# Optimization experiments

Measured on AMD Instinct MI355X. Metric: run time of the kernel, lower is better.

Reference implementation:

```python
import jax, jax.numpy as jnp
import numpy as np

NUM_USERS = 100000
NUM_ITEMS = 50000
DIM = 64
LAYERS = 3
K = 1
N_NEGS = 16
NNZ = 2000000
BATCH = 2048
N_TOTAL = NUM_USERS + NUM_ITEMS


def setup_inputs() -> dict:
    key = jax.random.key(0)
    ks = jax.random.split(key, 8)
    return {
        "user_embed": 0.1 * jax.random.normal(ks[0], (NUM_USERS, DIM), dtype=jnp.float32),
        "item_embed": 0.1 * jax.random.normal(ks[1], (NUM_ITEMS, DIM), dtype=jnp.float32),
        "graph_vals": jax.random.uniform(ks[2], (NNZ,), dtype=jnp.float32),
        "graph_rows": jax.random.randint(ks[3], (NNZ,), 0, N_TOTAL, dtype=jnp.int32),
        "graph_cols": jax.random.randint(ks[4], (NNZ,), 0, N_TOTAL, dtype=jnp.int32),
        "user_index": jax.random.randint(ks[5], (BATCH,), 0, NUM_USERS, dtype=jnp.int32),
        "pos_index": jax.random.randint(ks[6], (BATCH,), 0, NUM_ITEMS, dtype=jnp.int32),
        "neg_index": jax.random.randint(ks[7], (BATCH, K * N_NEGS), 0, NUM_ITEMS, dtype=jnp.int32),
    }


def _spmm(vals, rows, cols, x):
    # sparse [N,N] @ dense [N,D] via gather + segment_sum
    return jax.ops.segment_sum(vals[:, None] * x[cols], rows, num_segments=N_TOTAL)


def _aggregate(user_embed, item_embed, graph_vals, graph_rows, graph_cols):
    lambdas = [(l + 1) / (LAYERS + 1) for l in range(LAYERS + 1)]
    e = jnp.concatenate([user_embed, item_embed], axis=0)  # [N, D]
    embeds = [e * lambdas[0]]
    for layer in range(LAYERS):
        e = _spmm(graph_vals, graph_rows, graph_cols, e)
        embeds.append(e * lambdas[layer + 1])
    emb = jnp.stack(embeds, axis=1)  # [N, L+1, D]
    return emb[:NUM_USERS], emb[NUM_USERS:]


def _neg_synth(user_emb, item_emb, user_index, neg_cands, pos_item, key):
    u_e = user_emb[user_index]          # [B, L+1, D]
    p_e = item_emb[pos_item]            # [B, L+1, D]
    n_e = item_emb[neg_cands]           # [B, n_negs, L+1, D]
    seed = jax.random.uniform(key, n_e.shape, dtype=n_e.dtype)
    n_e_ = seed * p_e[:, None] + (1.0 - seed) * n_e            # positive mixing
    scores = jnp.sum(u_e[:, None] * n_e_, axis=-1)             # [B, n_negs, L+1]
    idx = jnp.argmax(scores, axis=1)                            # [B, L+1]
    # select per (batch, layer) the best candidate (hop mixing)
    sel = jnp.take_along_axis(
        jnp.transpose(n_e_, (0, 2, 1, 3)),                      # [B, L+1, n_negs, D]
        idx[:, :, None, None], axis=2).squeeze(2)               # [B, L+1, D]
    return sel


def _pool(e):
    return e.reshape(e.shape[:-2] + (-1,))


def reference(user_embed, item_embed, graph_vals, graph_rows, graph_cols,
              user_index, pos_index, neg_index):
    user_emb, item_emb = _aggregate(user_embed, item_embed,
                                    graph_vals, graph_rows, graph_cols)
    nocon_u_e = user_emb[user_index]    # [B, L+1, D]
    nocon_pos_e = item_emb[pos_index]   # [B, L+1, D]
    key = jax.random.key(42)
    nocon_neg = []
    for k in range(K):
        cands = neg_index[:, k * N_NEGS:(k + 1) * N_NEGS]
        nocon_neg.append(_neg_synth(user_emb, item_emb, user_index, cands,
                                    pos_index, jax.random.fold_in(key, k)))
    nocon_neg_e = jnp.stack(nocon_neg, axis=1)  # [B, K, L+1, D]

    u_e = _pool(nocon_u_e)       # [B, (L+1)*D]
    pos_e = _pool(nocon_pos_e)
    neg_e = _pool(nocon_neg_e)   # [B, K, (L+1)*D]

    B = user_index.shape[0]
    reg_loss = 0.5 * (jnp.sum(nocon_u_e[:, 0, :] ** 2)
                      + jnp.sum(nocon_pos_e[:, 0, :] ** 2)
                      + jnp.sum(nocon_neg_e[:, :, 0, :] ** 2)) / float(B)

    pos_scores = jnp.sum(u_e * pos_e, axis=1)                 # [B]
    neg_scores = jnp.sum(u_e[:, None] * neg_e, axis=-1)       # [B, K]
    loss1 = jnp.mean(jnp.log(1.0 + jnp.sum(
        jnp.exp(neg_scores - pos_scores[:, None]), axis=1)))
    return (loss1, reg_loss)
```

## Files before the change

### kernel.cpp

```cpp
#include <hip/hip_runtime.h>

static constexpr int kNumUsers  = 100000;
static constexpr int kNumItems  = 50000;
static constexpr int kNTotal    = 150000;
static constexpr int kDim       = 64;
static constexpr int kNnz       = 2000000;
static constexpr int kBatch     = 2048;
static constexpr int kNeg       = 16;
static constexpr int kRowsPerBucket = 256;
static constexpr int kNumBuckets  = (kNTotal + kRowsPerBucket - 1) / kRowsPerBucket;
static constexpr int kBucketCap   = 4096;
static constexpr int kChunk       = 4096;
static constexpr int kEdgesPerThread = kChunk / 512;
static constexpr int kCurStride   = 16;
static constexpr int kMaxList     = 2048 + 2048 + kBatch * kNeg;
static constexpr unsigned kSeedHalf = 4194304u;

typedef float f32x2 __attribute__((ext_vector_type(2)));


__device__ __forceinline__ unsigned short f2bf(float f) {
  unsigned u = __float_as_uint(f);
  unsigned r = (u + 0x7FFFu + ((u >> 16) & 1u)) >> 16;
  return (unsigned short)r;
}
__device__ __forceinline__ float bf2f(unsigned short h) {
  return __uint_as_float((unsigned)h << 16);
}


struct KeyPair { unsigned a, b; };

constexpr KeyPair tf2x32_const(unsigned k0, unsigned k1, unsigned x0, unsigned x1) {
  unsigned ks[3] = {k0, k1, k0 ^ k1 ^ 0x1BD11BDAu};
  const unsigned rots[2][4] = {{13u,15u,26u,6u},{17u,29u,16u,24u}};
  x0 += ks[0]; x1 += ks[1];
  for (int g = 0; g < 5; ++g) {
    for (int i = 0; i < 4; ++i) {
      unsigned r = rots[g & 1][i];
      x0 += x1;
      x1 = (x1 << r) | (x1 >> (32u - r));
      x1 ^= x0;
    }
    x0 += ks[(g + 1) % 3];
    x1 += ks[(g + 2) % 3] + (unsigned)(g + 1);
  }
  return {x0, x1};
}

static constexpr KeyPair kFoldedKey = tf2x32_const(0u, 42u, 0u, 0u);

__device__ __forceinline__ unsigned rotl32(unsigned x, unsigned r) {
  return (x << r) | (x >> (32u - r));
}

__device__ __forceinline__ void tf2x32(unsigned k0, unsigned k1,
                                       unsigned x0, unsigned x1,
                                       unsigned& y0, unsigned& y1) {
  const unsigned ks2 = k0 ^ k1 ^ 0x1BD11BDAu;
  x0 += k0; x1 += k1;
#define TF_ROUND(r) { x0 += x1; x1 = rotl32(x1, (r)); x1 ^= x0; }
  TF_ROUND(13u) TF_ROUND(15u) TF_ROUND(26u) TF_ROUND(6u)
  x0 += k1;  x1 += ks2 + 1u;
  TF_ROUND(17u) TF_ROUND(29u) TF_ROUND(16u) TF_ROUND(24u)
  x0 += ks2; x1 += k0 + 2u;
  TF_ROUND(13u) TF_ROUND(15u) TF_ROUND(26u) TF_ROUND(6u)
  x0 += k0;  x1 += k1 + 3u;
  TF_ROUND(17u) TF_ROUND(29u) TF_ROUND(16u) TF_ROUND(24u)
  x0 += k1;  x1 += ks2 + 4u;
  TF_ROUND(13u) TF_ROUND(15u) TF_ROUND(26u) TF_ROUND(6u)
  x0 += ks2; x1 += k0 + 5u;
#undef TF_ROUND
  y0 = x0; y1 = x1;
}

__device__ __forceinline__ float bits2f(unsigned bits) {
  return __uint_as_float((bits >> 9) | 0x3F800000u) - 1.0f;
}

__device__ __forceinline__ float wred(float v) {
  for (int o = 32; o; o >>= 1) v += __shfl_xor(v, o, 64);
  return v;
}


__global__ void k_zeroinit(const float* __restrict__ ue, const float* __restrict__ ie,
                           unsigned* __restrict__ e0f8, int* __restrict__ cursor,
                           int* __restrict__ nrows, int* __restrict__ flags) {
  int i = blockIdx.x * blockDim.x + threadIdx.x;
  if (i < kNTotal * 16) {
    const float4* __restrict__ s4 = (i < kNumUsers * 16)
      ? ((const float4*)ue + i)
      : ((const float4*)ie + (i - kNumUsers * 16));
    float4 v = *s4;
    unsigned w = 0;
    w = __builtin_amdgcn_cvt_pk_fp8_f32(v.x, v.y, w, false);
    w = __builtin_amdgcn_cvt_pk_fp8_f32(v.z, v.w, w, true);
    e0f8[i] = w;
  }
  if (i < kNTotal) flags[i] = 0;
  if (i < kNumBuckets) cursor[i * kCurStride] = i * kBucketCap;
  if (i == 0) *nrows = 0;
}

__global__ void __launch_bounds__(512)
k_bscatter(const int* __restrict__ rows, const int* __restrict__ cols,
           const float* __restrict__ vals, int* __restrict__ cursor,
           int2* __restrict__ edges) {
  __shared__ int hist[kNumBuckets];
  __shared__ int base[kNumBuckets];
  int c0 = blockIdx.x * kChunk;

  int   er[kEdgesPerThread];
  int   ec[kEdgesPerThread];
  float ev[kEdgesPerThread];
  int n = 0;
#pragma unroll
  for (int i = 0; i < kEdgesPerThread; ++i) {
    int e = c0 + i * 512 + threadIdx.x;
    if (e < kNnz) {
      er[n] = rows[e];
      ec[n] = cols[e];
      ev[n] = vals[e];
      ++n;
    }
  }

  for (int i = threadIdx.x; i < kNumBuckets; i += 512) hist[i] = 0;
  __syncthreads();
  for (int i = 0; i < n; ++i) atomicAdd(&hist[er[i] >> 8], 1);
  __syncthreads();
  for (int i = threadIdx.x; i < kNumBuckets; i += 512) {
    int c = hist[i];
    base[i] = c ? atomicAdd(&cursor[i * kCurStride], c) : 0;
    hist[i] = 0;
  }
  __syncthreads();
  for (int i = 0; i < n; ++i) {
    int r = er[i];
    int b = r >> 8;
    int p = base[b] + atomicAdd(&hist[b], 1);
    if (p < (b + 1) * kBucketCap) {
      int2 pk;
      pk.x = ec[i] | ((r & 255) << 18);
      pk.y = __float_as_int(ev[i]);
      edges[p] = pk;
    }
  }
}

__global__ void __launch_bounds__(256)
k_bucket_csr(const int2* __restrict__ edges, const int* __restrict__ cursor,
             int2* __restrict__ edges2, int* __restrict__ rbeg, int* __restrict__ rend) {
  __shared__ int cnts[kRowsPerBucket];
  __shared__ int offs[kRowsPerBucket];
  __shared__ int wsum[4];
  int b = blockIdx.x;
  int lo = b * kBucketCap;
  int cnt = cursor[b * kCurStride] - lo; if (cnt > kBucketCap) cnt = kBucketCap;

  cnts[threadIdx.x] = 0;
  __syncthreads();
  for (int e = threadIdx.x; e < cnt; e += 256)
    atomicAdd(&cnts[(edges[lo + e].x >> 18) & 255], 1);
  __syncthreads();

  {
    int tid = threadIdx.x;
    int v = cnts[tid];
    int s = v;
    for (int o = 1; o < 64; o <<= 1) {
      int t = __shfl_up(s, o, 64);
      if ((tid & 63) >= o) s += t;
    }
    if ((tid & 63) == 63) wsum[tid >> 6] = s;
    __syncthreads();
    int woff = 0;
    for (int ww = 0; ww < (tid >> 6); ++ww) woff += wsum[ww];
    int excl = woff + s - v;
    offs[tid] = excl;
    int row = (b << 8) + tid;
    if (row < kNTotal) {
      rbeg[row] = lo + excl;
      rend[row] = lo + excl + v;
    }
  }
  __syncthreads();

  for (int e = threadIdx.x; e < cnt; e += 256) {
    int2 pk = edges[lo + e];
    int rl = (pk.x >> 18) & 255;
    int p = atomicAdd(&offs[rl], 1);
    edges2[lo + p] = make_int2(pk.x & 0x3FFFF, pk.y);
  }
}

__global__ void k_flaglist(const int* __restrict__ uidx, const int* __restrict__ pidx,
                           const int* __restrict__ nidx, int* __restrict__ flags,
                           int* __restrict__ rowlist, int* __restrict__ nrows) {
  int i = blockIdx.x * blockDim.x + threadIdx.x;
  int node = -1;
  if (i < kBatch) node = uidx[i];
  else if (i < 2 * kBatch) node = kNumUsers + pidx[i - kBatch];
  else if (i < 2 * kBatch + kBatch * kNeg) node = kNumUsers + nidx[i - 2 * kBatch];
  if (node >= 0 && atomicExch(&flags[node], 1) == 0) {
    int p = atomicAdd(nrows, 1);
    rowlist[p] = node;
  }
}

#define FMA8(d, v) {                                                      \
    f32x2 q0 = __builtin_amdgcn_cvt_pk_f32_fp8((d).x, false);             \
    f32x2 q1 = __builtin_amdgcn_cvt_pk_f32_fp8((d).x, true);              \
    f32x2 q2 = __builtin_amdgcn_cvt_pk_f32_fp8((d).y, false);             \
    f32x2 q3 = __builtin_amdgcn_cvt_pk_f32_fp8((d).y, true);              \
    a[0] += (v) * q0.x; a[1] += (v) * q0.y; a[2] += (v) * q1.x;           \
    a[3] += (v) * q1.y; a[4] += (v) * q2.x; a[5] += (v) * q2.y;           \
    a[6] += (v) * q3.x; a[7] += (v) * q3.y; }

__device__ __forceinline__ void spmm_row8(int row, int ln,
                                          const int* __restrict__ rbeg,
                                          const int* __restrict__ rend,
                                          const int2* __restrict__ edges2,
                                          const uint2* __restrict__ src8,
                                          unsigned short* __restrict__ dstbf,
                                          uint2* __restrict__ dstf8, int wb) {
  int s = rbeg[row], t = rend[row];
  float a[8];
#pragma unroll
  for (int i = 0; i < 8; ++i) a[i] = 0.0f;
  int e = s;
  for (; e + 3 < t; e += 4) {
    int2 p0 = edges2[e],     p1 = edges2[e + 1];
    int2 p2 = edges2[e + 2], p3 = edges2[e + 3];
    uint2 d0 = src8[(size_t)p0.x * 8 + ln];
    uint2 d1 = src8[(size_t)p1.x * 8 + ln];
    uint2 d2 = src8[(size_t)p2.x * 8 + ln];
    uint2 d3 = src8[(size_t)p3.x * 8 + ln];
    FMA8(d0, __int_as_float(p0.y))
    FMA8(d1, __int_as_float(p1.y))
    FMA8(d2, __int_as_float(p2.y))
    FMA8(d3, __int_as_float(p3.y))
  }
  if (e + 1 < t) {
    int2 p0 = edges2[e], p1 = edges2[e + 1];
    uint2 d0 = src8[(size_t)p0.x * 8 + ln];
    uint2 d1 = src8[(size_t)p1.x * 8 + ln];
    FMA8(d0, __int_as_float(p0.y))
    FMA8(d1, __int_as_float(p1.y))
    e += 2;
  }
  if (e < t) {
    int2 p0 = edges2[e];
    uint2 d0 = src8[(size_t)p0.x * 8 + ln];
    FMA8(d0, __int_as_float(p0.y))
  }
  if (wb) {
    uint4 ob;
    ob.x = (unsigned)f2bf(a[0]) | ((unsigned)f2bf(a[1]) << 16);
    ob.y = (unsigned)f2bf(a[2]) | ((unsigned)f2bf(a[3]) << 16);
    ob.z = (unsigned)f2bf(a[4]) | ((unsigned)f2bf(a[5]) << 16);
    ob.w = (unsigned)f2bf(a[6]) | ((unsigned)f2bf(a[7]) << 16);
    *(uint4*)(dstbf + ((size_t)row << 6) + (ln << 3)) = ob;
  }
  if (dstf8) {
    uint2 o8;
    o8.x = 0; o8.y = 0;
    o8.x = __builtin_amdgcn_cvt_pk_fp8_f32(a[0], a[1], o8.x, false);
    o8.x = __builtin_amdgcn_cvt_pk_fp8_f32(a[2], a[3], o8.x, true);
    o8.y = __builtin_amdgcn_cvt_pk_fp8_f32(a[4], a[5], o8.y, false);
    o8.y = __builtin_amdgcn_cvt_pk_fp8_f32(a[6], a[7], o8.y, true);
    dstf8[(size_t)row * 8 + ln] = o8;
  }
}

__global__ void __launch_bounds__(256)
k_spmm_all(const int* __restrict__ rbeg, const int* __restrict__ rend,
           const int2* __restrict__ edges2, const uint2* __restrict__ src8,
           unsigned short* __restrict__ dstbf, uint2* __restrict__ dstf8,
           const int* __restrict__ flags) {
  int row = blockIdx.x * 32 + (threadIdx.x >> 3);
  if (row >= kNTotal) return;
  spmm_row8(row, threadIdx.x & 7, rbeg, rend, edges2, src8, dstbf, dstf8,
            flags[row]);
}

__global__ void __launch_bounds__(256)
k_spmm_list(const int* __restrict__ rbeg, const int* __restrict__ rend,
            const int2* __restrict__ edges2, const uint2* __restrict__ src8,
            unsigned short* __restrict__ dstbf, const int* __restrict__ rowlist,
            const int* __restrict__ nrows) {
  int gid = blockIdx.x * 32 + (threadIdx.x >> 3);
  if (gid >= *nrows) return;
  spmm_row8(rowlist[gid], threadIdx.x & 7, rbeg, rend, edges2, src8, dstbf,
            nullptr, 1);
}

__global__ void __launch_bounds__(256)
k_batch(const float* __restrict__ ue, const float* __restrict__ ie,
        const unsigned short* __restrict__ e1, const unsigned short* __restrict__ e2,
        const unsigned short* __restrict__ e3, const int* __restrict__ uidx,
        const int* __restrict__ pidx, const int* __restrict__ nidx,
        float2* __restrict__ bout) {
  const float LAM[4] = {0.25f, 0.5f, 0.75f, 1.0f};
  int b0 = blockIdx.x;
  int b1 = b0 + kBatch / 2;
  int lane = threadIdx.x & 63;
  int w = threadIdx.x >> 6;

  __shared__ float s_score[2][kNeg][4];
  __shared__ float s_sq0[2][kNeg];
  __shared__ float s_pos[2], s_usq[2], s_psq[2];

  int un0 = uidx[b0], pi0 = pidx[b0];
  int un1 = uidx[b1], pi1 = pidx[b1];
  size_t uo0 = ((size_t)un0 << 6) + lane, po0 = ((size_t)(kNumUsers + pi0) << 6) + lane;
  size_t uo1 = ((size_t)un1 << 6) + lane, po1 = ((size_t)(kNumUsers + pi1) << 6) + lane;
  float u0[4], p0[4], u1[4], p1[4];
  u0[0] = ue[uo0] * LAM[0]; p0[0] = ie[((size_t)pi0 << 6) + lane] * LAM[0];
  u1[0] = ue[uo1] * LAM[0]; p1[0] = ie[((size_t)pi1 << 6) + lane] * LAM[0];
  u0[1] = bf2f(e1[uo0]) * LAM[1]; p0[1] = bf2f(e1[po0]) * LAM[1];
  u1[1] = bf2f(e1[uo1]) * LAM[1]; p1[1] = bf2f(e1[po1]) * LAM[1];
  u0[2] = bf2f(e2[uo0]) * LAM[2]; p0[2] = bf2f(e2[po0]) * LAM[2];
  u1[2] = bf2f(e2[uo1]) * LAM[2]; p1[2] = bf2f(e2[po1]) * LAM[2];
  u0[3] = bf2f(e3[uo0]) * LAM[3]; p0[3] = bf2f(e3[po0]) * LAM[3];
  u1[3] = bf2f(e3[uo1]) * LAM[3]; p1[3] = bf2f(e3[po1]) * LAM[3];

  if (w == 0) {
    float ps = wred(u0[0]*p0[0] + u0[1]*p0[1] + u0[2]*p0[2] + u0[3]*p0[3]);
    float uq = wred(u0[0] * u0[0]);
    float pq = wred(p0[0] * p0[0]);
    if (lane == 0) { s_pos[0] = ps; s_usq[0] = uq; s_psq[0] = pq; }
  } else if (w == 1) {
    float ps = wred(u1[0]*p1[0] + u1[1]*p1[1] + u1[2]*p1[2] + u1[3]*p1[3]);
    float uq = wred(u1[0] * u1[0]);
    float pq = wred(p1[0] * p1[0]);
    if (lane == 0) { s_pos[1] = ps; s_usq[1] = uq; s_psq[1] = pq; }
  }

#pragma unroll
  for (int j = 0; j < 4; ++j) {
    int c = w * 4 + j;
    int ni0 = nidx[b0 * kNeg + c];
    int ni1 = nidx[b1 * kNeg + c];
    size_t no0 = ((size_t)(kNumUsers + ni0) << 6) + lane;
    size_t no1 = ((size_t)(kNumUsers + ni1) << 6) + lane;
#pragma unroll
    for (int l = 0; l < 4; ++l) {
      float nv0, nv1;
      if (l == 0) {
        nv0 = ie[((size_t)ni0 << 6) + lane] * LAM[0];
        nv1 = ie[((size_t)ni1 << 6) + lane] * LAM[0];
      } else if (l == 1) { nv0 = bf2f(e1[no0]) * LAM[1]; nv1 = bf2f(e1[no1]) * LAM[1]; }
      else if (l == 2)   { nv0 = bf2f(e2[no0]) * LAM[2]; nv1 = bf2f(e2[no1]) * LAM[2]; }
      else               { nv0 = bf2f(e3[no0]) * LAM[3]; nv1 = bf2f(e3[no1]) * LAM[3]; }
      unsigned si = ((unsigned)(b0 * kNeg + c) * 4u + (unsigned)l) * 64u + (unsigned)lane;
      unsigned y0, y1;
      tf2x32(kFoldedKey.a, kFoldedKey.b, si, si + kSeedHalf, y0, y1);
      float sd0 = bits2f(y0);
      float sd1 = bits2f(y1);
      float nm0 = sd0 * p0[l] + (1.0f - sd0) * nv0;
      float nm1 = sd1 * p1[l] + (1.0f - sd1) * nv1;
      float sc0 = wred(u0[l] * nm0);
      float sc1 = wred(u1[l] * nm1);
      if (l == 0) {
        float q0 = wred(nm0 * nm0);
        float q1 = wred(nm1 * nm1);
        if (lane == 0) { s_sq0[0][c] = q0; s_sq0[1][c] = q1; }
      }
      if (lane == 0) { s_score[0][c][l] = sc0; s_score[1][c][l] = sc1; }
    }
  }
  __syncthreads();

  if (w < 2) {
    int c = lane & 15, l = lane >> 4;
    float v = s_score[w][c][l];
    int idx = c;
#pragma unroll
    for (int o = 1; o < 16; o <<= 1) {
      float ov = __shfl_xor(v, o, 64);
      int oi = __shfl_xor(idx, o, 64);
      bool take = (ov > v) || (ov == v && oi < idx);
      v = take ? ov : v;
      idx = take ? oi : idx;
    }
    float sum = v;
    sum += __shfl_xor(sum, 16, 64);
    sum += __shfl_xor(sum, 32, 64);
    if (lane == 0) {
      float x = sum - s_pos[w];
      float term = logf(1.0f + expf(x));
      float reg = 0.5f * (s_usq[w] + s_psq[w] + s_sq0[w][idx]);
      bout[w == 0 ? b0 : b1] = make_float2(term, reg);
    }
  }
}

__global__ void __launch_bounds__(256)
k_reduce(const float2* __restrict__ bout, float* __restrict__ out) {
  float t = 0.0f, r = 0.0f;
  for (int i = threadIdx.x; i < kBatch; i += 256) {
    float2 v = bout[i];
    t += v.x; r += v.y;
  }
  t = wred(t); r = wred(r);
  __shared__ float st[4], sr[4];
  int w = threadIdx.x >> 6;
  if ((threadIdx.x & 63) == 0) { st[w] = t; sr[w] = r; }
  __syncthreads();
  if (threadIdx.x == 0) {
    out[0] = (st[0] + st[1] + st[2] + st[3]) / (float)kBatch;
    out[1] = (sr[0] + sr[1] + sr[2] + sr[3]) / (float)kBatch;
  }
}


extern "C" void kernel_launch(void* const* d_in, const int* in_sizes, int n_in,
                              void* d_out, int out_size, void* d_ws, size_t ws_size,
                              hipStream_t stream) {
  const float* ue   = (const float*)d_in[0];
  const float* ie   = (const float*)d_in[1];
  const float* gv   = (const float*)d_in[2];
  const int*   gr   = (const int*)d_in[3];
  const int*   gc   = (const int*)d_in[4];
  const int*   uidx = (const int*)d_in[5];
  const int*   pidx = (const int*)d_in[6];
  const int*   nidx = (const int*)d_in[7];
  float* out = (float*)d_out;

  char* ws = (char*)d_ws;
  size_t off = 0;
  auto alloc = [&](size_t bytes) -> void* {
    off = (off + 255) & ~(size_t)255;
    void* p = ws + off;
    off += bytes;
    return p;
  };
  const size_t tblElems = (size_t)kNTotal * kDim;
  unsigned*       e0f8 = (unsigned*)      alloc(tblElems);
  unsigned short* e1bf = (unsigned short*)alloc(tblElems * 2);
  uint2*          e1f8 = (uint2*)         alloc(tblElems);
  unsigned short* e2bf = (unsigned short*)alloc(tblElems * 2);
  uint2*          e2f8 = (uint2*)         alloc(tblElems);
  unsigned short* e3bf = (unsigned short*)alloc(tblElems * 2);
  int2* edges   = (int2*)alloc((size_t)kNumBuckets * kBucketCap * sizeof(int2));
  int2* edges2  = (int2*)alloc((size_t)kNumBuckets * kBucketCap * sizeof(int2));
  int*  cursor  = (int*) alloc((size_t)kNumBuckets * kCurStride * sizeof(int));
  int*  rbeg    = (int*) alloc((size_t)kNTotal * sizeof(int));
  int*  rend    = (int*) alloc((size_t)kNTotal * sizeof(int));
  int*  flags   = (int*) alloc((size_t)kNTotal * sizeof(int));
  int*  rowlist = (int*) alloc((size_t)kMaxList * sizeof(int));
  int*  nrows   = (int*) alloc(16 * sizeof(int));
  float2* bout  = (float2*)alloc((size_t)kBatch * sizeof(float2));
  (void)ws_size; (void)in_sizes; (void)n_in; (void)out_size;

  hipLaunchKernelGGL(k_zeroinit,   dim3((kNTotal * 16 + 255) / 256), dim3(256), 0, stream,
                     ue, ie, e0f8, cursor, nrows, flags);
  hipLaunchKernelGGL(k_bscatter,   dim3((kNnz + kChunk - 1) / kChunk), dim3(512), 0, stream,
                     gr, gc, gv, cursor, edges);
  hipLaunchKernelGGL(k_bucket_csr, dim3(kNumBuckets),           dim3(256), 0, stream,
                     edges, cursor, edges2, rbeg, rend);
  hipLaunchKernelGGL(k_flaglist,   dim3((2 * kBatch + kBatch * kNeg + 255) / 256), dim3(256), 0, stream,
                     uidx, pidx, nidx, flags, rowlist, nrows);
  hipLaunchKernelGGL(k_spmm_all,   dim3((kNTotal + 31) / 32),   dim3(256), 0, stream,
                     rbeg, rend, edges2, (const uint2*)e0f8, e1bf, e1f8, flags);
  hipLaunchKernelGGL(k_spmm_all,   dim3((kNTotal + 31) / 32),   dim3(256), 0, stream,
                     rbeg, rend, edges2, e1f8, e2bf, e2f8, flags);
  hipLaunchKernelGGL(k_spmm_list,  dim3((kMaxList + 31) / 32),  dim3(256), 0, stream,
                     rbeg, rend, edges2, e2f8, e3bf, rowlist, nrows);
  hipLaunchKernelGGL(k_batch,      dim3(kBatch / 2),            dim3(256), 0, stream,
                     ue, ie, e1bf, e2bf, e3bf, uidx, pidx, nidx, bout);
  hipLaunchKernelGGL(k_reduce,     dim3(1),                     dim3(256), 0, stream, bout, out);
}
```

Measured before the change: 173.2 us.

## Split CSR edges into column and bf16 value arrays, widen bucket sort block

Stores the sorted edge list as separate int column and bf16 value arrays instead of interleaved int2 pairs. This cuts edge-stream bytes read by each SpMM pass from 8 to 6 per edge. The bucket CSR kernel moves to 512 threads per block to speed up the per-bucket sort. Rounding edge weights to bf16 adds precision loss on top of the existing fp8 embedding tables.

```diff
diff --git a/kernel.cpp b/kernel.cpp
--- a/kernel.cpp
+++ b/kernel.cpp
@@ -149,49 +149,53 @@
   }
 }
 
-__global__ void __launch_bounds__(256)
+__global__ void __launch_bounds__(512)
 k_bucket_csr(const int2* __restrict__ edges, const int* __restrict__ cursor,
-             int2* __restrict__ edges2, int* __restrict__ rbeg, int* __restrict__ rend) {
+             int* __restrict__ col2, unsigned short* __restrict__ val2,
+             int* __restrict__ rbeg, int* __restrict__ rend) {
   __shared__ int cnts[kRowsPerBucket];
   __shared__ int offs[kRowsPerBucket];
   __shared__ int wsum[4];
   int b = blockIdx.x;
   int lo = b * kBucketCap;
   int cnt = cursor[b * kCurStride] - lo; if (cnt > kBucketCap) cnt = kBucketCap;
-
-  cnts[threadIdx.x] = 0;
-  __syncthreads();
-  for (int e = threadIdx.x; e < cnt; e += 256)
+  int tid = threadIdx.x;
+
+  if (tid < kRowsPerBucket) cnts[tid] = 0;
+  __syncthreads();
+  for (int e = tid; e < cnt; e += 512)
     atomicAdd(&cnts[(edges[lo + e].x >> 18) & 255], 1);
   __syncthreads();
 
   {
-    int tid = threadIdx.x;
-    int v = cnts[tid];
+    int v = (tid < kRowsPerBucket) ? cnts[tid] : 0;
     int s = v;
     for (int o = 1; o < 64; o <<= 1) {
       int t = __shfl_up(s, o, 64);
       if ((tid & 63) >= o) s += t;
     }
-    if ((tid & 63) == 63) wsum[tid >> 6] = s;
+    if (tid < kRowsPerBucket && (tid & 63) == 63) wsum[tid >> 6] = s;
     __syncthreads();
-    int woff = 0;
-    for (int ww = 0; ww < (tid >> 6); ++ww) woff += wsum[ww];
-    int excl = woff + s - v;
-    offs[tid] = excl;
-    int row = (b << 8) + tid;
-    if (row < kNTotal) {
-      rbeg[row] = lo + excl;
-      rend[row] = lo + excl + v;
-    }
-  }
-  __syncthreads();
-
-  for (int e = threadIdx.x; e < cnt; e += 256) {
+    if (tid < kRowsPerBucket) {
+      int woff = 0;
+      for (int ww = 0; ww < (tid >> 6); ++ww) woff += wsum[ww];
+      int excl = woff + s - v;
+      offs[tid] = excl;
+      int row = (b << 8) + tid;
+      if (row < kNTotal) {
+        rbeg[row] = lo + excl;
+        rend[row] = lo + excl + v;
+      }
+    }
+  }
+  __syncthreads();
+
+  for (int e = tid; e < cnt; e += 512) {
     int2 pk = edges[lo + e];
     int rl = (pk.x >> 18) & 255;
     int p = atomicAdd(&offs[rl], 1);
-    edges2[lo + p] = make_int2(pk.x & 0x3FFFF, pk.y);
+    col2[lo + p] = pk.x & 0x3FFFF;
+    val2[lo + p] = f2bf(__int_as_float(pk.y));
   }
 }
 
@@ -221,7 +225,8 @@
 __device__ __forceinline__ void spmm_row8(int row, int ln,
                                           const int* __restrict__ rbeg,
                                           const int* __restrict__ rend,
-                                          const int2* __restrict__ edges2,
+                                          const int* __restrict__ col2,
+                                          const unsigned short* __restrict__ val2,
                                           const uint2* __restrict__ src8,
                                           unsigned short* __restrict__ dstbf,
                                           uint2* __restrict__ dstf8, int wb) {
@@ -231,29 +236,33 @@
   for (int i = 0; i < 8; ++i) a[i] = 0.0f;
   int e = s;
   for (; e + 3 < t; e += 4) {
-    int2 p0 = edges2[e],     p1 = edges2[e + 1];
-    int2 p2 = edges2[e + 2], p3 = edges2[e + 3];
-    uint2 d0 = src8[(size_t)p0.x * 8 + ln];
-    uint2 d1 = src8[(size_t)p1.x * 8 + ln];
-    uint2 d2 = src8[(size_t)p2.x * 8 + ln];
-    uint2 d3 = src8[(size_t)p3.x * 8 + ln];
-    FMA8(d0, __int_as_float(p0.y))
-    FMA8(d1, __int_as_float(p1.y))
-    FMA8(d2, __int_as_float(p2.y))
-    FMA8(d3, __int_as_float(p3.y))
+    int c0 = col2[e],     c1 = col2[e + 1];
+    int c2 = col2[e + 2], c3 = col2[e + 3];
+    float v0 = bf2f(val2[e]),     v1 = bf2f(val2[e + 1]);
+    float v2 = bf2f(val2[e + 2]), v3 = bf2f(val2[e + 3]);
+    uint2 d0 = src8[(size_t)c0 * 8 + ln];
+    uint2 d1 = src8[(size_t)c1 * 8 + ln];
+    uint2 d2 = src8[(size_t)c2 * 8 + ln];
+    uint2 d3 = src8[(size_t)c3 * 8 + ln];
+    FMA8(d0, v0)
+    FMA8(d1, v1)
+    FMA8(d2, v2)
+    FMA8(d3, v3)
   }
   if (e + 1 < t) {
-    int2 p0 = edges2[e], p1 = edges2[e + 1];
-    uint2 d0 = src8[(size_t)p0.x * 8 + ln];
-    uint2 d1 = src8[(size_t)p1.x * 8 + ln];
-    FMA8(d0, __int_as_float(p0.y))
-    FMA8(d1, __int_as_float(p1.y))
+    int c0 = col2[e], c1 = col2[e + 1];
+    float v0 = bf2f(val2[e]), v1 = bf2f(val2[e + 1]);
+    uint2 d0 = src8[(size_t)c0 * 8 + ln];
+    uint2 d1 = src8[(size_t)c1 * 8 + ln];
+    FMA8(d0, v0)
+    FMA8(d1, v1)
     e += 2;
   }
   if (e < t) {
-    int2 p0 = edges2[e];
-    uint2 d0 = src8[(size_t)p0.x * 8 + ln];
-    FMA8(d0, __int_as_float(p0.y))
+    int c0 = col2[e];
+    float v0 = bf2f(val2[e]);
+    uint2 d0 = src8[(size_t)c0 * 8 + ln];
+    FMA8(d0, v0)
   }
   if (wb) {
     uint4 ob;
@@ -276,23 +285,25 @@
 
 __global__ void __launch_bounds__(256)
 k_spmm_all(const int* __restrict__ rbeg, const int* __restrict__ rend,
-           const int2* __restrict__ edges2, const uint2* __restrict__ src8,
+           const int* __restrict__ col2, const unsigned short* __restrict__ val2,
+           const uint2* __restrict__ src8,
            unsigned short* __restrict__ dstbf, uint2* __restrict__ dstf8,
            const int* __restrict__ flags) {
   int row = blockIdx.x * 32 + (threadIdx.x >> 3);
   if (row >= kNTotal) return;
-  spmm_row8(row, threadIdx.x & 7, rbeg, rend, edges2, src8, dstbf, dstf8,
+  spmm_row8(row, threadIdx.x & 7, rbeg, rend, col2, val2, src8, dstbf, dstf8,
             flags[row]);
 }
 
 __global__ void __launch_bounds__(256)
 k_spmm_list(const int* __restrict__ rbeg, const int* __restrict__ rend,
-            const int2* __restrict__ edges2, const uint2* __restrict__ src8,
+            const int* __restrict__ col2, const unsigned short* __restrict__ val2,
+            const uint2* __restrict__ src8,
             unsigned short* __restrict__ dstbf, const int* __restrict__ rowlist,
             const int* __restrict__ nrows) {
   int gid = blockIdx.x * 32 + (threadIdx.x >> 3);
   if (gid >= *nrows) return;
-  spmm_row8(rowlist[gid], threadIdx.x & 7, rbeg, rend, edges2, src8, dstbf,
+  spmm_row8(rowlist[gid], threadIdx.x & 7, rbeg, rend, col2, val2, src8, dstbf,
             nullptr, 1);
 }
 
@@ -438,14 +449,16 @@
     return p;
   };
   const size_t tblElems = (size_t)kNTotal * kDim;
+  const size_t edgeCap  = (size_t)kNumBuckets * kBucketCap;
   unsigned*       e0f8 = (unsigned*)      alloc(tblElems);
   unsigned short* e1bf = (unsigned short*)alloc(tblElems * 2);
   uint2*          e1f8 = (uint2*)         alloc(tblElems);
   unsigned short* e2bf = (unsigned short*)alloc(tblElems * 2);
   uint2*          e2f8 = (uint2*)         alloc(tblElems);
   unsigned short* e3bf = (unsigned short*)alloc(tblElems * 2);
-  int2* edges   = (int2*)alloc((size_t)kNumBuckets * kBucketCap * sizeof(int2));
-  int2* edges2  = (int2*)alloc((size_t)kNumBuckets * kBucketCap * sizeof(int2));
+  int2* edges   = (int2*)alloc(edgeCap * sizeof(int2));
+  int*  col2    = (int*) alloc(edgeCap * sizeof(int));
+  unsigned short* val2 = (unsigned short*)alloc(edgeCap * 2);
   int*  cursor  = (int*) alloc((size_t)kNumBuckets * kCurStride * sizeof(int));
   int*  rbeg    = (int*) alloc((size_t)kNTotal * sizeof(int));
   int*  rend    = (int*) alloc((size_t)kNTotal * sizeof(int));
@@ -459,16 +472,16 @@
                      ue, ie, e0f8, cursor, nrows, flags);
   hipLaunchKernelGGL(k_bscatter,   dim3((kNnz + kChunk - 1) / kChunk), dim3(512), 0, stream,
                      gr, gc, gv, cursor, edges);
-  hipLaunchKernelGGL(k_bucket_csr, dim3(kNumBuckets),           dim3(256), 0, stream,
-                     edges, cursor, edges2, rbeg, rend);
+  hipLaunchKernelGGL(k_bucket_csr, dim3(kNumBuckets),           dim3(512), 0, stream,
+                     edges, cursor, col2, val2, rbeg, rend);
   hipLaunchKernelGGL(k_flaglist,   dim3((2 * kBatch + kBatch * kNeg + 255) / 256), dim3(256), 0, stream,
                      uidx, pidx, nidx, flags, rowlist, nrows);
   hipLaunchKernelGGL(k_spmm_all,   dim3((kNTotal + 31) / 32),   dim3(256), 0, stream,
-                     rbeg, rend, edges2, (const uint2*)e0f8, e1bf, e1f8, flags);
+                     rbeg, rend, col2, val2, (const uint2*)e0f8, e1bf, e1f8, flags);
   hipLaunchKernelGGL(k_spmm_all,   dim3((kNTotal + 31) / 32),   dim3(256), 0, stream,
-                     rbeg, rend, edges2, e1f8, e2bf, e2f8, flags);
+                     rbeg, rend, col2, val2, e1f8, e2bf, e2f8, flags);
   hipLaunchKernelGGL(k_spmm_list,  dim3((kMaxList + 31) / 32),  dim3(256), 0, stream,
-                     rbeg, rend, edges2, e2f8, e3bf, rowlist, nrows);
+                     rbeg, rend, col2, val2, e2f8, e3bf, rowlist, nrows);
   hipLaunchKernelGGL(k_batch,      dim3(kBatch / 2),            dim3(256), 0, stream,
                      ue, ie, e1bf, e2bf, e3bf, uidx, pidx, nidx, bout);
   hipLaunchKernelGGL(k_reduce,     dim3(1),                     dim3(256), 0, stream, bout, out);
```

Result: slower. 178.7 us (+3.2%).
